# Performance work log

Hardware: AMD Instinct MI355X
Metric: run time of the kernel (lower is better)

The kernel has to match this reference:

```python
import jax, jax.numpy as jnp
import numpy as np
import math

DIM = 1024
NUM_HEADS = 16
HEAD_DIM = DIM // NUM_HEADS
B, S = 2, 2048

def setup_inputs() -> dict:
    key = jax.random.key(0)
    ks = jax.random.split(key, 9)
    sc = 0.02
    return {
        "x": jax.random.normal(ks[0], (B, S, DIM), jnp.float32),
        "Wq": jax.random.normal(ks[1], (DIM, DIM), jnp.float32) * sc,
        "bq": jax.random.normal(ks[2], (DIM,), jnp.float32) * sc,
        "Wk": jax.random.normal(ks[3], (DIM, DIM), jnp.float32) * sc,
        "bk": jax.random.normal(ks[4], (DIM,), jnp.float32) * sc,
        "Wv": jax.random.normal(ks[5], (DIM, DIM), jnp.float32) * sc,
        "bv": jax.random.normal(ks[6], (DIM,), jnp.float32) * sc,
        "Wo": jax.random.normal(ks[7], (DIM, DIM), jnp.float32) * sc,
        "bo": jax.random.normal(ks[8], (DIM,), jnp.float32) * sc,
    }

def reference(x, Wq, bq, Wk, bk, Wv, bv, Wo, bo):
    b, s, d = x.shape
    h, hd = NUM_HEADS, HEAD_DIM
    # qkv projections: [B,S,D] -> [B,H,S,hd]
    def split_heads(t):
        return t.reshape(b, s, h, hd).transpose(0, 2, 1, 3)
    q = split_heads(x @ Wq + bq)
    k = split_heads(x @ Wk + bk)
    v = split_heads(x @ Wv + bv)
    # scores [B,H,S,S], scale, causal mask via where(-10000), softmax
    scores = jnp.einsum('bhqd,bhkd->bhqk', q, k) / math.sqrt(hd)
    causal = jnp.tril(jnp.ones((s, s), dtype=bool))  # [S,S]
    scores = jnp.where(causal[None, None], scores, jnp.asarray(-10000.0, scores.dtype))
    probs = jax.nn.softmax(scores, axis=-1)
    ctx = jnp.einsum('bhqk,bhkd->bhqd', probs, v)
    ctx = ctx.transpose(0, 2, 1, 3).reshape(b, s, d)
    return ctx @ Wo + bo
```

## Files before the change

kernel.cpp:

```cpp
#include <hip/hip_runtime.h>
#include <hip/hip_bf16.h>

#define DIM 1024
#define NUM_HEADS 16
#define HEAD_DIM 64
#define BATCH 2
#define SEQ 2048
#define M_ROWS (BATCH * SEQ)

typedef short bh8 __attribute__((ext_vector_type(8)));
typedef float f32x4 __attribute__((ext_vector_type(4)));
typedef float f32x16 __attribute__((ext_vector_type(16)));

#define SCALE_Q 0.18033688011116016f

#define MFMA16(a, b, c) __builtin_amdgcn_mfma_f32_16x16x32_bf16(a, b, c, 0, 0, 0)
#define MFMA32(a, b, c) __builtin_amdgcn_mfma_f32_32x32x16_bf16(a, b, c, 0, 0, 0)

#if __has_builtin(__builtin_amdgcn_exp2f)
#define EXP2F(x) __builtin_amdgcn_exp2f(x)
#else
#define EXP2F(x) exp2f(x)
#endif

__device__ __forceinline__ ushort f2bf(float f) {
    union { float f; unsigned u; } v; v.f = f;
    unsigned u = v.u;
    unsigned r = (u + 0x7FFFu + ((u >> 16) & 1u)) >> 16;
    return (ushort)r;
}

__device__ __forceinline__ unsigned cvt_pk_bf16(float lo, float hi) {
    unsigned r;
    asm("v_cvt_pk_bf16_f32 %0, %1, %2" : "=v"(r) : "v"(lo), "v"(hi));
    return r;
}

__device__ __forceinline__ void plane_swap(unsigned a, unsigned b,
                                           unsigned& o0, unsigned& o1, int h) {
#if __has_builtin(__builtin_amdgcn_permlane32_swap)
    (void)h;
    auto pr = __builtin_amdgcn_permlane32_swap(a, b, false, false);
    unsigned o[2]; __builtin_memcpy(o, &pr, 8);
    o0 = o[0]; o1 = o[1];
#else
    unsigned sa = (unsigned)__shfl_xor((int)a, 32);
    unsigned sb = (unsigned)__shfl_xor((int)b, 32);
    o0 = h ? sb : a;
    o1 = h ? b : sa;
#endif
}

__device__ __forceinline__ void async_cp16(const ushort* g, ushort* l) {
    __builtin_amdgcn_global_load_lds(
        (const __attribute__((address_space(1))) void*)(uintptr_t)g,
        (__attribute__((address_space(3))) void*)(uint32_t)(uintptr_t)l,
        16, 0, 0);
}

__global__ __launch_bounds__(256) void prep_inputs(
    const float* __restrict__ W0, const float* __restrict__ W1,
    const float* __restrict__ W2, const float* __restrict__ W3,
    const float* __restrict__ x,
    ushort* __restrict__ T0, ushort* __restrict__ T1,
    ushort* __restrict__ T2, ushort* __restrict__ T3,
    ushort* __restrict__ xb)
{
    const int z = blockIdx.z;
    const int t = threadIdx.x;
    if (z == 4) {
        int base = (blockIdx.y * 32 + blockIdx.x) * 1024 + t;
        const float4* in4 = (const float4*)x;
        ushort4* out4 = (ushort4*)xb;
        #pragma unroll
        for (int i = 0; i < 4; ++i) {
            float4 v = in4[base + i * 256];
            ushort4 o;
            o.x = f2bf(v.x); o.y = f2bf(v.y); o.z = f2bf(v.z); o.w = f2bf(v.w);
            out4[base + i * 256] = o;
        }
        return;
    }
    __shared__ float tile[32][33];
    const float* W = (z == 0) ? W0 : (z == 1) ? W1 : (z == 2) ? W2 : W3;
    ushort* Wt = (z == 0) ? T0 : (z == 1) ? T1 : (z == 2) ? T2 : T3;
    const int tx = t & 31, ty = t >> 5;
    const int k0 = blockIdx.y * 32, n0 = blockIdx.x * 32;
    #pragma unroll
    for (int i = 0; i < 4; ++i)
        tile[ty + 8 * i][tx] = W[(size_t)(k0 + ty + 8 * i) * DIM + n0 + tx];
    __syncthreads();
    #pragma unroll
    for (int i = 0; i < 4; ++i)
        Wt[(size_t)(n0 + ty + 8 * i) * DIM + k0 + tx] = f2bf(tile[tx][ty + 8 * i]);
}

__device__ __forceinline__ void gemm_core128(
    const ushort* __restrict__ A, const ushort* __restrict__ Bt,
    ushort* smem, int m0, int n0, int t, f32x4 acc[4][4])
{
    ushort* As = smem;
    ushort* Bs = smem + 8192;
    const int lane = t & 63, wave = t >> 6;
    const int col = lane & 15, quad = lane >> 4;
    const int wm = (wave & 1) * 64, wn = (wave >> 1) * 64;

    for (int k0 = 0; k0 < DIM; k0 += 64) {
        __syncthreads();
        #pragma unroll
        for (int j = 0; j < 4; ++j) {
            int C = wave * 256 + j * 64 + lane;
            int row = C >> 3;
            int lch = (C & 7) ^ (row & 7);
            async_cp16(&A[(size_t)(m0 + row) * DIM + k0 + lch * 8],
                       &As[(wave * 256 + j * 64) * 8]);
        }
        #pragma unroll
        for (int j = 0; j < 4; ++j) {
            int C = wave * 256 + j * 64 + lane;
            int row = C >> 3;
            int lch = (C & 7) ^ (row & 7);
            async_cp16(&Bt[(size_t)(n0 + row) * DIM + k0 + lch * 8],
                       &Bs[(wave * 256 + j * 64) * 8]);
        }
        __syncthreads();
        #pragma unroll
        for (int kk = 0; kk < 2; ++kk) {
            bh8 af[4], bfr[4];
            #pragma unroll
            for (int mi = 0; mi < 4; ++mi) {
                int row = wm + mi * 16 + col;
                af[mi] = *(const bh8*)&As[row * 64 + (((kk * 4 + quad) ^ (row & 7)) * 8)];
            }
            #pragma unroll
            for (int ni = 0; ni < 4; ++ni) {
                int row = wn + ni * 16 + col;
                bfr[ni] = *(const bh8*)&Bs[row * 64 + (((kk * 4 + quad) ^ (row & 7)) * 8)];
            }
            #pragma unroll
            for (int mi = 0; mi < 4; ++mi)
                #pragma unroll
                for (int ni = 0; ni < 4; ++ni)
                    acc[mi][ni] = MFMA16(af[mi], bfr[ni], acc[mi][ni]);
        }
    }
}

__device__ __forceinline__ void gemm_core64(
    const ushort* __restrict__ A, const ushort* __restrict__ Bt,
    ushort* smem, int m0, int n0, int t, f32x4 acc[4][2])
{
    ushort* As = smem;
    ushort* Bs = smem + 8192;
    const int lane = t & 63, wave = t >> 6;
    const int col = lane & 15, quad = lane >> 4;
    const int wm = (wave & 1) * 64, wn = (wave >> 1) * 32;

    for (int k0 = 0; k0 < DIM; k0 += 64) {
        __syncthreads();
        #pragma unroll
        for (int j = 0; j < 4; ++j) {
            int C = wave * 256 + j * 64 + lane;
            int row = C >> 3;
            int lch = (C & 7) ^ (row & 7);
            async_cp16(&A[(size_t)(m0 + row) * DIM + k0 + lch * 8],
                       &As[(wave * 256 + j * 64) * 8]);
        }
        #pragma unroll
        for (int j = 0; j < 2; ++j) {
            int C = wave * 128 + j * 64 + lane;
            int row = C >> 3;
            int lch = (C & 7) ^ (row & 7);
            async_cp16(&Bt[(size_t)(n0 + row) * DIM + k0 + lch * 8],
                       &Bs[(wave * 128 + j * 64) * 8]);
        }
        __syncthreads();
        #pragma unroll
        for (int kk = 0; kk < 2; ++kk) {
            bh8 af[4], bfr[2];
            #pragma unroll
            for (int mi = 0; mi < 4; ++mi) {
                int row = wm + mi * 16 + col;
                af[mi] = *(const bh8*)&As[row * 64 + (((kk * 4 + quad) ^ (row & 7)) * 8)];
            }
            #pragma unroll
            for (int ni = 0; ni < 2; ++ni) {
                int row = wn + ni * 16 + col;
                bfr[ni] = *(const bh8*)&Bs[row * 64 + (((kk * 4 + quad) ^ (row & 7)) * 8)];
            }
            #pragma unroll
            for (int mi = 0; mi < 4; ++mi)
                #pragma unroll
                for (int ni = 0; ni < 2; ++ni)
                    acc[mi][ni] = MFMA16(af[mi], bfr[ni], acc[mi][ni]);
        }
    }
}

__global__ __launch_bounds__(256) void gemm_qkv(
    const ushort* __restrict__ A,
    const ushort* __restrict__ WqT, const ushort* __restrict__ WkT,
    const ushort* __restrict__ WvT,
    const float* __restrict__ bq, const float* __restrict__ bk,
    const float* __restrict__ bv,
    ushort* __restrict__ qo, ushort* __restrict__ ko_, ushort* __restrict__ vo)
{
    __shared__ ushort smem[17408];
    const int z = blockIdx.z;
    const ushort* Bt = (z == 0) ? WqT : (z == 1) ? WkT : WvT;
    const float* bias = (z == 0) ? bq : (z == 1) ? bk : bv;
    ushort* outp = (z == 0) ? qo : (z == 1) ? ko_ : vo;

    const int t = threadIdx.x;
    const int lane = t & 63, wave = t >> 6;
    const int col = lane & 15, quad = lane >> 4;
    const int m0 = blockIdx.y * 128, n0 = blockIdx.x * 128;
    const int wm = (wave & 1) * 64, wn = (wave >> 1) * 64;
    f32x4 acc[4][4] = {};

    gemm_core128(A, Bt, smem, m0, n0, t, acc);

    const int b = m0 >> 11, s0 = m0 & (SEQ - 1);

    if (z < 2) {
        const float scl = (z == 0) ? SCALE_Q : 1.f;
        __syncthreads();
        ushort* LT = smem;
        #pragma unroll
        for (int mi = 0; mi < 4; ++mi)
            #pragma unroll
            for (int ni = 0; ni < 4; ++ni) {
                int dl = wn + ni * 16 + col;
                float bvv = bias[n0 + dl];
                #pragma unroll
                for (int r = 0; r < 4; ++r) {
                    int ml = wm + mi * 16 + quad * 4 + r;
                    LT[ml * 136 + dl] = f2bf((acc[mi][ni][r] + bvv) * scl);
                }
            }
        __syncthreads();
        #pragma unroll
        for (int i = 0; i < 8; ++i) {
            int c = i * 256 + t;
            int row = c >> 4, cg = (c & 15) * 8;
            int hh = (n0 + cg) >> 6, d = (n0 + cg) & 63;
            *(uint4*)&outp[((size_t)(b * NUM_HEADS + hh) * SEQ + s0 + row) * HEAD_DIM + d] =
                *(const uint4*)&LT[row * 136 + cg];
        }
    } else {
        __syncthreads();
        ushort* LT = smem;
        #pragma unroll
        for (int mi = 0; mi < 4; ++mi)
            #pragma unroll
            for (int ni = 0; ni < 4; ++ni) {
                int nl = wn + ni * 16 + col;
                float bvv = bias[n0 + nl];
                #pragma unroll
                for (int r = 0; r < 4; ++r) {
                    int ml = wm + mi * 16 + quad * 4 + r;
                    LT[nl * 136 + ml] = f2bf(acc[mi][ni][r] + bvv);
                }
            }
        __syncthreads();
        #pragma unroll
        for (int i = 0; i < 8; ++i) {
            int c = i * 256 + t;
            int drow = c >> 4, mo = (c & 15) * 8;
            int hh = (n0 + drow) >> 6, d = (n0 + drow) & 63;
            *(uint4*)&outp[(((size_t)(b * NUM_HEADS + hh) * HEAD_DIM + d) << 11) + s0 + mo] =
                *(const uint4*)&LT[drow * 136 + mo];
        }
    }
}

__global__ __launch_bounds__(256) void gemm_out(
    const ushort* __restrict__ A, const ushort* __restrict__ Bt,
    const float* __restrict__ bias, float* __restrict__ C)
{
    __shared__ ushort smem[12288];
    const int t = threadIdx.x;
    const int lane = t & 63, wave = t >> 6;
    const int col = lane & 15, quad = lane >> 4;
    const int m0 = blockIdx.y * 128, n0 = blockIdx.x * 64;
    const int wm = (wave & 1) * 64, wn = (wave >> 1) * 32;
    f32x4 acc[4][2] = {};

    gemm_core64(A, Bt, smem, m0, n0, t, acc);

    #pragma unroll
    for (int mi = 0; mi < 4; ++mi)
        #pragma unroll
        for (int ni = 0; ni < 2; ++ni) {
            int n = n0 + wn + ni * 16 + col;
            float bvv = bias[n];
            #pragma unroll
            for (int r = 0; r < 4; ++r) {
                int m = m0 + wm + mi * 16 + quad * 4 + r;
                C[(size_t)m * DIM + n] = acc[mi][ni][r] + bvv;
            }
        }
}

__global__ __launch_bounds__(256, 2) void attn_mfma(
    const ushort* __restrict__ Qg, const ushort* __restrict__ Kg,
    const ushort* __restrict__ Vtg, ushort* __restrict__ ctx)
{
    __shared__ char smem[34304];
    float* OA   = (float*)smem;
    float* OB   = (float*)(smem + 16640);
    float* lbuf = (float*)(smem + 33280);

    const int t = threadIdx.x;
    const int lane = t & 63, wave = t >> 6;
    const int q32 = lane & 31, h = lane >> 5;
    const int bh = blockIdx.x & 31;
    const int pi = blockIdx.x >> 5;
    const int b = bh >> 4, hd = bh & 15;
    const int kw0 = wave * 32;
    const ushort* Kp = Kg + ((size_t)bh << 17);
    const ushort* Vp = Vtg + ((size_t)bh << 17);
    const ushort* Qp0 = Qg + ((size_t)bh << 17);

    #pragma unroll 1
    for (int ph = 0; ph < 2; ++ph) {
        const int qt = ph ? pi : (31 - pi);
        const int q0 = qt << 6;

        bh8 qf[2][4];
        #pragma unroll
        for (int qti = 0; qti < 2; ++qti)
            #pragma unroll
            for (int kc = 0; kc < 4; ++kc)
                qf[qti][kc] = *(const bh8*)&Qp0[((size_t)(q0 + qti * 32 + q32) << 6)
                                                + kc * 16 + h * 8];

        f32x16 O[2][2] = {};
        float l[2] = {0.f, 0.f};
        const int nIter = (q0 + 191) >> 7;

        bh8 kf_n[4], vf_n[2][2];
        #pragma unroll
        for (int kc = 0; kc < 4; ++kc)
            kf_n[kc] = *(const bh8*)&Kp[((size_t)(kw0 + q32) << 6) + kc * 16 + h * 8];
        #pragma unroll
        for (int dti = 0; dti < 2; ++dti)
            #pragma unroll
            for (int kc = 0; kc < 2; ++kc)
                vf_n[dti][kc] = *(const bh8*)&Vp[((size_t)(dti * 32 + q32) << 11)
                                                 + kw0 + kc * 16 + h * 8];

        #pragma unroll 1
        for (int it = 0; it < nIter; ++it) {
            const int kb = it << 7;
            bh8 kf[4], vf[2][2];
            #pragma unroll
            for (int kc = 0; kc < 4; ++kc) kf[kc] = kf_n[kc];
            #pragma unroll
            for (int dti = 0; dti < 2; ++dti) {
                vf[dti][0] = vf_n[dti][0]; vf[dti][1] = vf_n[dti][1];
            }

            if (it + 1 < nIter) {
                const int kb2 = kb + 128;
                #pragma unroll
                for (int kc = 0; kc < 4; ++kc)
                    kf_n[kc] = *(const bh8*)&Kp[((size_t)(kb2 + kw0 + q32) << 6)
                                                + kc * 16 + h * 8];
                #pragma unroll
                for (int dti = 0; dti < 2; ++dti)
                    #pragma unroll
                    for (int kc = 0; kc < 2; ++kc)
                        vf_n[dti][kc] = *(const bh8*)&Vp[((size_t)(dti * 32 + q32) << 11)
                                                         + kb2 + kw0 + kc * 16 + h * 8];
            }

            if (kb + kw0 > q0 + 63) continue;

            f32x16 St[2] = {};
            #pragma unroll
            for (int kc = 0; kc < 4; ++kc) {
                St[0] = MFMA32(kf[kc], qf[0][kc], St[0]);
                St[1] = MFMA32(kf[kc], qf[1][kc], St[1]);
            }

            if (kb + kw0 + 31 > q0) {
                #pragma unroll
                for (int qti = 0; qti < 2; ++qti) {
                    int q_abs = q0 + qti * 32 + q32;
                    #pragma unroll
                    for (int r = 0; r < 16; ++r) {
                        int key_abs = kb + kw0 + (r & 3) + ((r >> 2) << 3) + 4 * h;
                        if (key_abs > q_abs) St[qti][r] = -1e30f;
                    }
                }
            }

            #pragma unroll
            for (int qti = 0; qti < 2; ++qti) {
                float p[16];
                #pragma unroll
                for (int r = 0; r < 16; ++r) p[r] = EXP2F(St[qti][r]);
                float t0 = (p[0] + p[1]) + (p[2] + p[3]);
                float t1 = (p[4] + p[5]) + (p[6] + p[7]);
                float t2 = (p[8] + p[9]) + (p[10] + p[11]);
                float t3 = (p[12] + p[13]) + (p[14] + p[15]);
                l[qti] += (t0 + t1) + (t2 + t3);

                unsigned w[8];
                #pragma unroll
                for (int m = 0; m < 8; ++m) w[m] = cvt_pk_bf16(p[2 * m], p[2 * m + 1]);
                unsigned j0, j1, j2, j3, j4, j5, j6, j7;
                plane_swap(w[0], w[2], j0, j2, h);
                plane_swap(w[1], w[3], j1, j3, h);
                plane_swap(w[4], w[6], j4, j6, h);
                plane_swap(w[5], w[7], j5, j7, h);
                union { unsigned u[4]; bh8 v; } pu0, pu1;
                pu0.u[0] = j0; pu0.u[1] = j1; pu0.u[2] = j2; pu0.u[3] = j3;
                pu1.u[0] = j4; pu1.u[1] = j5; pu1.u[2] = j6; pu1.u[3] = j7;

                O[qti][0] = MFMA32(vf[0][0], pu0.v, O[qti][0]);
                O[qti][1] = MFMA32(vf[1][0], pu0.v, O[qti][1]);
                O[qti][0] = MFMA32(vf[0][1], pu1.v, O[qti][0]);
                O[qti][1] = MFMA32(vf[1][1], pu1.v, O[qti][1]);
            }
        }

        l[0] += __shfl_xor(l[0], 32);
        l[1] += __shfl_xor(l[1], 32);
        if (lane < 32) {
            lbuf[wave * 64 + q32]      = l[0];
            lbuf[wave * 64 + 32 + q32] = l[1];
        }
        __syncthreads();

        if (wave == 1 || wave == 3) {
            float* dst = (wave == 1) ? OA : OB;
            #pragma unroll
            for (int qti = 0; qti < 2; ++qti)
                #pragma unroll
                for (int dti = 0; dti < 2; ++dti)
                    #pragma unroll
                    for (int r = 0; r < 16; ++r) {
                        int d_l = dti * 32 + (r & 3) + ((r >> 2) << 3) + 4 * h;
                        dst[d_l * 65 + qti * 32 + q32] = O[qti][dti][r];
                    }
        }
        __syncthreads();
        if (wave == 0 || wave == 2) {
            float* src = (wave == 0) ? OA : OB;
            #pragma unroll
            for (int qti = 0; qti < 2; ++qti)
                #pragma unroll
                for (int dti = 0; dti < 2; ++dti)
                    #pragma unroll
                    for (int r = 0; r < 16; ++r) {
                        int d_l = dti * 32 + (r & 3) + ((r >> 2) << 3) + 4 * h;
                        O[qti][dti][r] += src[d_l * 65 + qti * 32 + q32];
                    }
        }
        __syncthreads();
        if (wave == 2) {
            #pragma unroll
            for (int qti = 0; qti < 2; ++qti)
                #pragma unroll
                for (int dti = 0; dti < 2; ++dti)
                    #pragma unroll
                    for (int r = 0; r < 16; ++r) {
                        int d_l = dti * 32 + (r & 3) + ((r >> 2) << 3) + 4 * h;
                        OA[d_l * 65 + qti * 32 + q32] = O[qti][dti][r];
                    }
        }
        __syncthreads();
        if (wave == 0) {
            float tot0 = lbuf[q32] + lbuf[64 + q32] + lbuf[128 + q32] + lbuf[192 + q32];
            float tot1 = lbuf[32 + q32] + lbuf[96 + q32] + lbuf[160 + q32] + lbuf[224 + q32];
            float inv0 = 1.f / tot0, inv1 = 1.f / tot1;
            ushort* Oq = (ushort*)(smem + 16640);
            #pragma unroll
            for (int qti = 0; qti < 2; ++qti) {
                float invq = qti ? inv1 : inv0;
                int qrow = qti * 32 + q32;
                #pragma unroll
                for (int dti = 0; dti < 2; ++dti)
                    #pragma unroll
                    for (int rg = 0; rg < 4; ++rg) {
                        int d0 = dti * 32 + rg * 8 + 4 * h;
                        float s0 = (O[qti][dti][rg * 4 + 0] + OA[(d0 + 0) * 65 + qrow]) * invq;
                        float s1 = (O[qti][dti][rg * 4 + 1] + OA[(d0 + 1) * 65 + qrow]) * invq;
                        float s2 = (O[qti][dti][rg * 4 + 2] + OA[(d0 + 2) * 65 + qrow]) * invq;
                        float s3 = (O[qti][dti][rg * 4 + 3] + OA[(d0 + 3) * 65 + qrow]) * invq;
                        uint2 pk; pk.x = cvt_pk_bf16(s0, s1); pk.y = cvt_pk_bf16(s2, s3);
                        *(uint2*)&Oq[qrow * 72 + d0] = pk;
                    }
            }
            #pragma unroll
            for (int i = 0; i < 8; ++i) {
                int c = i * 64 + lane;
                int row = c >> 3, ko = (c & 7) * 8;
                *(uint4*)&ctx[((size_t)(b * SEQ) + q0 + row) * DIM + (hd << 6) + ko] =
                    *(const uint4*)&Oq[row * 72 + ko];
            }
        }
        __syncthreads();
    }
}

extern "C" void kernel_launch(void* const* d_in, const int* in_sizes, int n_in,
                              void* d_out, int out_size, void* d_ws, size_t ws_size,
                              hipStream_t stream) {
    const float* x  = (const float*)d_in[0];
    const float* Wq = (const float*)d_in[1];
    const float* bq = (const float*)d_in[2];
    const float* Wk = (const float*)d_in[3];
    const float* bk = (const float*)d_in[4];
    const float* Wv = (const float*)d_in[5];
    const float* bv = (const float*)d_in[6];
    const float* Wo = (const float*)d_in[7];
    const float* bo = (const float*)d_in[8];
    float* out = (float*)d_out;

    ushort* x_bf   = (ushort*)d_ws;
    ushort* wq_t   = x_bf + 4194304;
    ushort* wk_t   = wq_t + 1048576;
    ushort* wv_t   = wk_t + 1048576;
    ushort* wo_t   = wv_t + 1048576;
    ushort* q_ws   = wo_t + 1048576;
    ushort* k_ws   = q_ws + 4194304;
    ushort* vt_ws  = k_ws + 4194304;
    ushort* ctx_ws = vt_ws + 4194304;

    dim3 pgrid(32, 32, 5);
    prep_inputs<<<pgrid, 256, 0, stream>>>(Wq, Wk, Wv, Wo, x,
                                           wq_t, wk_t, wv_t, wo_t, x_bf);

    dim3 qkv_grid(DIM / 128, M_ROWS / 128, 3);
    gemm_qkv<<<qkv_grid, 256, 0, stream>>>(x_bf, wq_t, wk_t, wv_t,
                                           bq, bk, bv, q_ws, k_ws, vt_ws);

    attn_mfma<<<512, 256, 0, stream>>>(q_ws, k_ws, vt_ws, ctx_ws);

    dim3 ogrid(DIM / 64, M_ROWS / 128);
    gemm_out<<<ogrid, 256, 0, stream>>>(ctx_ws, wo_t, bo, out);
}
```

Before: 201.7 us.

## Split attention into one q-tile per block, add MFMA priority and GEMM block swizzle

The attention kernel previously paired a long and a short causal q-tile per block for load balance. Now it launches 1024 blocks with one q-tile each, ordered heaviest first, and exits the loop early instead of skipping masked iterations. It also raises wave priority around the MFMA sections and remaps block indices in both GEMM kernels to group blocks that share operand tiles for better L2 reuse. The risk is worse tail balance without the pairing, and the early break also drops the prefetch that skipped iterations used to issue.

```diff
diff --git a/kernel.cpp b/kernel.cpp
--- a/kernel.cpp
+++ b/kernel.cpp
@@ -146,7 +146,10 @@
     }
 }
 
-__device__ __forceinline__ void gemm_core64(
+#define GTM 128
+#define GTN 64
+
+__device__ __forceinline__ void gemm_core(
     const ushort* __restrict__ A, const ushort* __restrict__ Bt,
     ushort* smem, int m0, int n0, int t, f32x4 acc[4][2])
 {
@@ -206,7 +209,10 @@
     ushort* __restrict__ qo, ushort* __restrict__ ko_, ushort* __restrict__ vo)
 {
     __shared__ ushort smem[17408];
-    const int z = blockIdx.z;
+    const int lin = blockIdx.x + 8 * blockIdx.y + 256 * blockIdx.z;
+    const int swz = (lin & 7) * 96 + (lin >> 3);
+    const int bx = swz & 7, by = (swz >> 3) & 31, z = swz >> 8;
+
     const ushort* Bt = (z == 0) ? WqT : (z == 1) ? WkT : WvT;
     const float* bias = (z == 0) ? bq : (z == 1) ? bk : bv;
     ushort* outp = (z == 0) ? qo : (z == 1) ? ko_ : vo;
@@ -214,7 +220,7 @@
     const int t = threadIdx.x;
     const int lane = t & 63, wave = t >> 6;
     const int col = lane & 15, quad = lane >> 4;
-    const int m0 = blockIdx.y * 128, n0 = blockIdx.x * 128;
+    const int m0 = by * 128, n0 = bx * 128;
     const int wm = (wave & 1) * 64, wn = (wave >> 1) * 64;
     f32x4 acc[4][4] = {};
 
@@ -279,14 +285,18 @@
     const float* __restrict__ bias, float* __restrict__ C)
 {
     __shared__ ushort smem[12288];
+    const int lin = blockIdx.x + 16 * blockIdx.y;
+    const int swz = (lin & 7) * 64 + (lin >> 3);
+    const int bx = swz & 15, by = swz >> 4;
+
     const int t = threadIdx.x;
     const int lane = t & 63, wave = t >> 6;
     const int col = lane & 15, quad = lane >> 4;
-    const int m0 = blockIdx.y * 128, n0 = blockIdx.x * 64;
+    const int m0 = by * GTM, n0 = bx * GTN;
     const int wm = (wave & 1) * 64, wn = (wave >> 1) * 32;
     f32x4 acc[4][2] = {};
 
-    gemm_core64(A, Bt, smem, m0, n0, t, acc);
+    gemm_core(A, Bt, smem, m0, n0, t, acc);
 
     #pragma unroll
     for (int mi = 0; mi < 4; ++mi)
@@ -315,194 +325,192 @@
     const int lane = t & 63, wave = t >> 6;
     const int q32 = lane & 31, h = lane >> 5;
     const int bh = blockIdx.x & 31;
-    const int pi = blockIdx.x >> 5;
+    const int qt = 31 - (blockIdx.x >> 5);
     const int b = bh >> 4, hd = bh & 15;
+    const int q0 = qt << 6;
     const int kw0 = wave * 32;
     const ushort* Kp = Kg + ((size_t)bh << 17);
     const ushort* Vp = Vtg + ((size_t)bh << 17);
-    const ushort* Qp0 = Qg + ((size_t)bh << 17);
+    const ushort* Qp = Qg + ((size_t)bh << 17);
+
+    bh8 qf[2][4];
+    #pragma unroll
+    for (int qti = 0; qti < 2; ++qti)
+        #pragma unroll
+        for (int kc = 0; kc < 4; ++kc)
+            qf[qti][kc] = *(const bh8*)&Qp[((size_t)(q0 + qti * 32 + q32) << 6)
+                                           + kc * 16 + h * 8];
+
+    f32x16 O[2][2] = {};
+    float l[2] = {0.f, 0.f};
+    const int nIter = (q0 + 191) >> 7;
+
+    bh8 kf_n[4], vf_n[2][2];
+    #pragma unroll
+    for (int kc = 0; kc < 4; ++kc)
+        kf_n[kc] = *(const bh8*)&Kp[((size_t)(kw0 + q32) << 6) + kc * 16 + h * 8];
+    #pragma unroll
+    for (int dti = 0; dti < 2; ++dti)
+        #pragma unroll
+        for (int kc = 0; kc < 2; ++kc)
+            vf_n[dti][kc] = *(const bh8*)&Vp[((size_t)(dti * 32 + q32) << 11)
+                                             + kw0 + kc * 16 + h * 8];
 
     #pragma unroll 1
-    for (int ph = 0; ph < 2; ++ph) {
-        const int qt = ph ? pi : (31 - pi);
-        const int q0 = qt << 6;
-
-        bh8 qf[2][4];
+    for (int it = 0; it < nIter; ++it) {
+        const int kb = it << 7;
+        if (kb + kw0 > q0 + 63) break;
+
+        bh8 kf[4], vf[2][2];
+        #pragma unroll
+        for (int kc = 0; kc < 4; ++kc) kf[kc] = kf_n[kc];
+        #pragma unroll
+        for (int dti = 0; dti < 2; ++dti) {
+            vf[dti][0] = vf_n[dti][0]; vf[dti][1] = vf_n[dti][1];
+        }
+
+        const int kb2 = kb + 128;
+        if (it + 1 < nIter) {
+            #pragma unroll
+            for (int kc = 0; kc < 4; ++kc)
+                kf_n[kc] = *(const bh8*)&Kp[((size_t)(kb2 + kw0 + q32) << 6)
+                                            + kc * 16 + h * 8];
+            #pragma unroll
+            for (int dti = 0; dti < 2; ++dti)
+                #pragma unroll
+                for (int kc = 0; kc < 2; ++kc)
+                    vf_n[dti][kc] = *(const bh8*)&Vp[((size_t)(dti * 32 + q32) << 11)
+                                                     + kb2 + kw0 + kc * 16 + h * 8];
+        }
+
+        f32x16 St[2] = {};
+        __builtin_amdgcn_s_setprio(1);
+        #pragma unroll
+        for (int kc = 0; kc < 4; ++kc) {
+            St[0] = MFMA32(kf[kc], qf[0][kc], St[0]);
+            St[1] = MFMA32(kf[kc], qf[1][kc], St[1]);
+        }
+        __builtin_amdgcn_s_setprio(0);
+
+        if (kb + kw0 + 31 > q0) {
+            #pragma unroll
+            for (int qti = 0; qti < 2; ++qti) {
+                int q_abs = q0 + qti * 32 + q32;
+                #pragma unroll
+                for (int r = 0; r < 16; ++r) {
+                    int key_abs = kb + kw0 + (r & 3) + ((r >> 2) << 3) + 4 * h;
+                    if (key_abs > q_abs) St[qti][r] = -1e30f;
+                }
+            }
+        }
+
+        #pragma unroll
+        for (int qti = 0; qti < 2; ++qti) {
+            float p[16];
+            #pragma unroll
+            for (int r = 0; r < 16; ++r) p[r] = EXP2F(St[qti][r]);
+            float t0 = (p[0] + p[1]) + (p[2] + p[3]);
+            float t1 = (p[4] + p[5]) + (p[6] + p[7]);
+            float t2 = (p[8] + p[9]) + (p[10] + p[11]);
+            float t3 = (p[12] + p[13]) + (p[14] + p[15]);
+            l[qti] += (t0 + t1) + (t2 + t3);
+
+            unsigned w[8];
+            #pragma unroll
+            for (int m = 0; m < 8; ++m) w[m] = cvt_pk_bf16(p[2 * m], p[2 * m + 1]);
+            unsigned j0, j1, j2, j3, j4, j5, j6, j7;
+            plane_swap(w[0], w[2], j0, j2, h);
+            plane_swap(w[1], w[3], j1, j3, h);
+            plane_swap(w[4], w[6], j4, j6, h);
+            plane_swap(w[5], w[7], j5, j7, h);
+            union { unsigned u[4]; bh8 v; } pu0, pu1;
+            pu0.u[0] = j0; pu0.u[1] = j1; pu0.u[2] = j2; pu0.u[3] = j3;
+            pu1.u[0] = j4; pu1.u[1] = j5; pu1.u[2] = j6; pu1.u[3] = j7;
+
+            __builtin_amdgcn_s_setprio(1);
+            O[qti][0] = MFMA32(vf[0][0], pu0.v, O[qti][0]);
+            O[qti][1] = MFMA32(vf[1][0], pu0.v, O[qti][1]);
+            O[qti][0] = MFMA32(vf[0][1], pu1.v, O[qti][0]);
+            O[qti][1] = MFMA32(vf[1][1], pu1.v, O[qti][1]);
+            __builtin_amdgcn_s_setprio(0);
+        }
+    }
+
+    l[0] += __shfl_xor(l[0], 32);
+    l[1] += __shfl_xor(l[1], 32);
+    if (lane < 32) {
+        lbuf[wave * 64 + q32]      = l[0];
+        lbuf[wave * 64 + 32 + q32] = l[1];
+    }
+    __syncthreads();
+
+    if (wave == 1 || wave == 3) {
+        float* dst = (wave == 1) ? OA : OB;
         #pragma unroll
         for (int qti = 0; qti < 2; ++qti)
             #pragma unroll
-            for (int kc = 0; kc < 4; ++kc)
-                qf[qti][kc] = *(const bh8*)&Qp0[((size_t)(q0 + qti * 32 + q32) << 6)
-                                                + kc * 16 + h * 8];
-
-        f32x16 O[2][2] = {};
-        float l[2] = {0.f, 0.f};
-        const int nIter = (q0 + 191) >> 7;
-
-        bh8 kf_n[4], vf_n[2][2];
-        #pragma unroll
-        for (int kc = 0; kc < 4; ++kc)
-            kf_n[kc] = *(const bh8*)&Kp[((size_t)(kw0 + q32) << 6) + kc * 16 + h * 8];
-        #pragma unroll
-        for (int dti = 0; dti < 2; ++dti)
-            #pragma unroll
-            for (int kc = 0; kc < 2; ++kc)
-                vf_n[dti][kc] = *(const bh8*)&Vp[((size_t)(dti * 32 + q32) << 11)
-                                                 + kw0 + kc * 16 + h * 8];
-
-        #pragma unroll 1
-        for (int it = 0; it < nIter; ++it) {
-            const int kb = it << 7;
-            bh8 kf[4], vf[2][2];
-            #pragma unroll
-            for (int kc = 0; kc < 4; ++kc) kf[kc] = kf_n[kc];
-            #pragma unroll
-            for (int dti = 0; dti < 2; ++dti) {
-                vf[dti][0] = vf_n[dti][0]; vf[dti][1] = vf_n[dti][1];
-            }
-
-            if (it + 1 < nIter) {
-                const int kb2 = kb + 128;
-                #pragma unroll
-                for (int kc = 0; kc < 4; ++kc)
-                    kf_n[kc] = *(const bh8*)&Kp[((size_t)(kb2 + kw0 + q32) << 6)
-                                                + kc * 16 + h * 8];
-                #pragma unroll
-                for (int dti = 0; dti < 2; ++dti)
-                    #pragma unroll
-                    for (int kc = 0; kc < 2; ++kc)
-                        vf_n[dti][kc] = *(const bh8*)&Vp[((size_t)(dti * 32 + q32) << 11)
-                                                         + kb2 + kw0 + kc * 16 + h * 8];
-            }
-
-            if (kb + kw0 > q0 + 63) continue;
-
-            f32x16 St[2] = {};
-            #pragma unroll
-            for (int kc = 0; kc < 4; ++kc) {
-                St[0] = MFMA32(kf[kc], qf[0][kc], St[0]);
-                St[1] = MFMA32(kf[kc], qf[1][kc], St[1]);
-            }
-
-            if (kb + kw0 + 31 > q0) {
-                #pragma unroll
-                for (int qti = 0; qti < 2; ++qti) {
-                    int q_abs = q0 + qti * 32 + q32;
-                    #pragma unroll
-                    for (int r = 0; r < 16; ++r) {
-                        int key_abs = kb + kw0 + (r & 3) + ((r >> 2) << 3) + 4 * h;
-                        if (key_abs > q_abs) St[qti][r] = -1e30f;
-                    }
-                }
-            }
-
-            #pragma unroll
-            for (int qti = 0; qti < 2; ++qti) {
-                float p[16];
-                #pragma unroll
-                for (int r = 0; r < 16; ++r) p[r] = EXP2F(St[qti][r]);
-                float t0 = (p[0] + p[1]) + (p[2] + p[3]);
-                float t1 = (p[4] + p[5]) + (p[6] + p[7]);
-                float t2 = (p[8] + p[9]) + (p[10] + p[11]);
-                float t3 = (p[12] + p[13]) + (p[14] + p[15]);
-                l[qti] += (t0 + t1) + (t2 + t3);
-
-                unsigned w[8];
-                #pragma unroll
-                for (int m = 0; m < 8; ++m) w[m] = cvt_pk_bf16(p[2 * m], p[2 * m + 1]);
-                unsigned j0, j1, j2, j3, j4, j5, j6, j7;
-                plane_swap(w[0], w[2], j0, j2, h);
-                plane_swap(w[1], w[3], j1, j3, h);
-                plane_swap(w[4], w[6], j4, j6, h);
-                plane_swap(w[5], w[7], j5, j7, h);
-                union { unsigned u[4]; bh8 v; } pu0, pu1;
-                pu0.u[0] = j0; pu0.u[1] = j1; pu0.u[2] = j2; pu0.u[3] = j3;
-                pu1.u[0] = j4; pu1.u[1] = j5; pu1.u[2] = j6; pu1.u[3] = j7;
-
-                O[qti][0] = MFMA32(vf[0][0], pu0.v, O[qti][0]);
-                O[qti][1] = MFMA32(vf[1][0], pu0.v, O[qti][1]);
-                O[qti][0] = MFMA32(vf[0][1], pu1.v, O[qti][0]);
-                O[qti][1] = MFMA32(vf[1][1], pu1.v, O[qti][1]);
-            }
-        }
-
-        l[0] += __shfl_xor(l[0], 32);
-        l[1] += __shfl_xor(l[1], 32);
-        if (lane < 32) {
-            lbuf[wave * 64 + q32]      = l[0];
-            lbuf[wave * 64 + 32 + q32] = l[1];
-        }
-        __syncthreads();
-
-        if (wave == 1 || wave == 3) {
-            float* dst = (wave == 1) ? OA : OB;
-            #pragma unroll
-            for (int qti = 0; qti < 2; ++qti)
-                #pragma unroll
-                for (int dti = 0; dti < 2; ++dti)
-                    #pragma unroll
-                    for (int r = 0; r < 16; ++r) {
-                        int d_l = dti * 32 + (r & 3) + ((r >> 2) << 3) + 4 * h;
-                        dst[d_l * 65 + qti * 32 + q32] = O[qti][dti][r];
-                    }
-        }
-        __syncthreads();
-        if (wave == 0 || wave == 2) {
-            float* src = (wave == 0) ? OA : OB;
-            #pragma unroll
-            for (int qti = 0; qti < 2; ++qti)
-                #pragma unroll
-                for (int dti = 0; dti < 2; ++dti)
-                    #pragma unroll
-                    for (int r = 0; r < 16; ++r) {
-                        int d_l = dti * 32 + (r & 3) + ((r >> 2) << 3) + 4 * h;
-                        O[qti][dti][r] += src[d_l * 65 + qti * 32 + q32];
-                    }
-        }
-        __syncthreads();
-        if (wave == 2) {
-            #pragma unroll
-            for (int qti = 0; qti < 2; ++qti)
-                #pragma unroll
-                for (int dti = 0; dti < 2; ++dti)
-                    #pragma unroll
-                    for (int r = 0; r < 16; ++r) {
-                        int d_l = dti * 32 + (r & 3) + ((r >> 2) << 3) + 4 * h;
-                        OA[d_l * 65 + qti * 32 + q32] = O[qti][dti][r];
-                    }
-        }
-        __syncthreads();
-        if (wave == 0) {
-            float tot0 = lbuf[q32] + lbuf[64 + q32] + lbuf[128 + q32] + lbuf[192 + q32];
-            float tot1 = lbuf[32 + q32] + lbuf[96 + q32] + lbuf[160 + q32] + lbuf[224 + q32];
-            float inv0 = 1.f / tot0, inv1 = 1.f / tot1;
-            ushort* Oq = (ushort*)(smem + 16640);
-            #pragma unroll
-            for (int qti = 0; qti < 2; ++qti) {
-                float invq = qti ? inv1 : inv0;
-                int qrow = qti * 32 + q32;
-                #pragma unroll
-                for (int dti = 0; dti < 2; ++dti)
-                    #pragma unroll
-                    for (int rg = 0; rg < 4; ++rg) {
-                        int d0 = dti * 32 + rg * 8 + 4 * h;
-                        float s0 = (O[qti][dti][rg * 4 + 0] + OA[(d0 + 0) * 65 + qrow]) * invq;
-                        float s1 = (O[qti][dti][rg * 4 + 1] + OA[(d0 + 1) * 65 + qrow]) * invq;
-                        float s2 = (O[qti][dti][rg * 4 + 2] + OA[(d0 + 2) * 65 + qrow]) * invq;
-                        float s3 = (O[qti][dti][rg * 4 + 3] + OA[(d0 + 3) * 65 + qrow]) * invq;
-                        uint2 pk; pk.x = cvt_pk_bf16(s0, s1); pk.y = cvt_pk_bf16(s2, s3);
-                        *(uint2*)&Oq[qrow * 72 + d0] = pk;
-                    }
-            }
-            #pragma unroll
-            for (int i = 0; i < 8; ++i) {
-                int c = i * 64 + lane;
-                int row = c >> 3, ko = (c & 7) * 8;
-                *(uint4*)&ctx[((size_t)(b * SEQ) + q0 + row) * DIM + (hd << 6) + ko] =
-                    *(const uint4*)&Oq[row * 72 + ko];
-            }
-        }
-        __syncthreads();
+            for (int dti = 0; dti < 2; ++dti)
+                #pragma unroll
+                for (int r = 0; r < 16; ++r) {
+                    int d_l = dti * 32 + (r & 3) + ((r >> 2) << 3) + 4 * h;
+                    dst[d_l * 65 + qti * 32 + q32] = O[qti][dti][r];
+                }
+    }
+    __syncthreads();
+    if (wave == 0 || wave == 2) {
+        float* src = (wave == 0) ? OA : OB;
+        #pragma unroll
+        for (int qti = 0; qti < 2; ++qti)
+            #pragma unroll
+            for (int dti = 0; dti < 2; ++dti)
+                #pragma unroll
+                for (int r = 0; r < 16; ++r) {
+                    int d_l = dti * 32 + (r & 3) + ((r >> 2) << 3) + 4 * h;
+                    O[qti][dti][r] += src[d_l * 65 + qti * 32 + q32];
+                }
+    }
+    __syncthreads();
+    if (wave == 2) {
+        #pragma unroll
+        for (int qti = 0; qti < 2; ++qti)
+            #pragma unroll
+            for (int dti = 0; dti < 2; ++dti)
+                #pragma unroll
+                for (int r = 0; r < 16; ++r) {
+                    int d_l = dti * 32 + (r & 3) + ((r >> 2) << 3) + 4 * h;
+                    OA[d_l * 65 + qti * 32 + q32] = O[qti][dti][r];
+                }
+    }
+    __syncthreads();
+    if (wave == 0) {
+        float tot0 = lbuf[q32] + lbuf[64 + q32] + lbuf[128 + q32] + lbuf[192 + q32];
+        float tot1 = lbuf[32 + q32] + lbuf[96 + q32] + lbuf[160 + q32] + lbuf[224 + q32];
+        float inv0 = 1.f / tot0, inv1 = 1.f / tot1;
+        ushort* Oq = (ushort*)(smem + 16640);
+        #pragma unroll
+        for (int qti = 0; qti < 2; ++qti) {
+            float invq = qti ? inv1 : inv0;
+            int qrow = qti * 32 + q32;
+            #pragma unroll
+            for (int dti = 0; dti < 2; ++dti)
+                #pragma unroll
+                for (int rg = 0; rg < 4; ++rg) {
+                    int d0 = dti * 32 + rg * 8 + 4 * h;
+                    float s0 = (O[qti][dti][rg * 4 + 0] + OA[(d0 + 0) * 65 + qrow]) * invq;
+                    float s1 = (O[qti][dti][rg * 4 + 1] + OA[(d0 + 1) * 65 + qrow]) * invq;
+                    float s2 = (O[qti][dti][rg * 4 + 2] + OA[(d0 + 2) * 65 + qrow]) * invq;
+                    float s3 = (O[qti][dti][rg * 4 + 3] + OA[(d0 + 3) * 65 + qrow]) * invq;
+                    uint2 pk; pk.x = cvt_pk_bf16(s0, s1); pk.y = cvt_pk_bf16(s2, s3);
+                    *(uint2*)&Oq[qrow * 72 + d0] = pk;
+                }
+        }
+        #pragma unroll
+        for (int i = 0; i < 8; ++i) {
+            int c = i * 64 + lane;
+            int row = c >> 3, ko = (c & 7) * 8;
+            *(uint4*)&ctx[((size_t)(b * SEQ) + q0 + row) * DIM + (hd << 6) + ko] =
+                *(const uint4*)&Oq[row * 72 + ko];
+        }
     }
 }
 
@@ -538,8 +546,8 @@
     gemm_qkv<<<qkv_grid, 256, 0, stream>>>(x_bf, wq_t, wk_t, wv_t,
                                            bq, bk, bv, q_ws, k_ws, vt_ws);
 
-    attn_mfma<<<512, 256, 0, stream>>>(q_ws, k_ws, vt_ws, ctx_ws);
-
-    dim3 ogrid(DIM / 64, M_ROWS / 128);
+    attn_mfma<<<1024, 256, 0, stream>>>(q_ws, k_ws, vt_ws, ctx_ws);
+
+    dim3 ogrid(DIM / GTN, M_ROWS / GTM);
     gemm_out<<<ogrid, 256, 0, stream>>>(ctx_ws, wo_t, bo, out);
 }
```

Result: faster. 191.9 us (-4.9%).
